# Optimization experiments

Measured on AMD Instinct MI355X. Metric: run time of the kernel, lower is better.

## Reference

```python
import jax, jax.numpy as jnp
import numpy as np

H, D = 16, 64  # num_attention_heads, attention_head_size
BASE = 10000.0

def _rope(q, k, seq_len):
    # RotaryPositionalEmbedding: inv_freq over arange(0, D, 2); emb = cat(freqs, freqs)
    inv_freq = 1.0 / (BASE ** (jnp.arange(0, D, 2, dtype=jnp.float32) / D))  # [D/2]=32
    pos = jnp.arange(seq_len, dtype=jnp.float32)
    freqs = jnp.outer(pos, inv_freq)            # [S, 32]; equals cos_emb[..., :d]
    cos, sin = jnp.cos(freqs), jnp.sin(freqs)   # [S, 32]
    d = D // 2                                   # 32: only first half of head dim rotated
    half = d // 2                                # 16: internal rotate-half within rot part
    def rot(x):  # x: [B, H, S, D]
        xr, xp = x[..., :d], x[..., d:]
        swapped = jnp.concatenate([xr[..., half:], xr[..., :half]], axis=-1)
        xr2 = xr * cos - swapped * sin
        return jnp.concatenate([xr2, xp], axis=-1)
    return rot(q), rot(k)

def setup_inputs() -> dict:
    key = jax.random.key(0)
    ks = jax.random.split(key, 9)
    B, S, E = 2, 2048, 1024
    std = 0.02  # initializer_range
    inp = {"hidden_states": jax.random.normal(ks[0], (B, S, E), jnp.float32)}
    for i, n in enumerate(["q", "k", "v", "d"]):
        inp[f"W{n}"] = jax.random.normal(ks[1 + 2 * i], (E, E), jnp.float32) * std
        inp[f"b{n}"] = jnp.zeros((E,), jnp.float32)
    return inp

def reference(hidden_states, Wq, bq, Wk, bk, Wv, bv, Wd, bd):
    B, S, E = hidden_states.shape
    def heads(x):  # [B,S,E] -> [B,H,S,D]
        return x.reshape(B, S, H, D).transpose(0, 2, 1, 3)
    q = heads(hidden_states @ Wq + bq)
    k = heads(hidden_states @ Wk + bk)
    v = heads(hidden_states @ Wv + bv)
    q, k = _rope(q, k, S)
    scores = jnp.einsum("bhqd,bhkd->bhqk", q, k) / jnp.sqrt(jnp.float32(D))
    causal = jnp.tril(jnp.ones((S, S), dtype=bool))
    scores = jnp.where(causal, scores, -jnp.inf)
    probs = jax.nn.softmax(scores, axis=-1)
    ctx = jnp.einsum("bhqk,bhkd->bhqd", probs, v)
    ctx = ctx.transpose(0, 2, 1, 3).reshape(B, S, E)
    return ctx @ Wd + bd
```

## Files before the change

### kernel.cpp

```cpp
#include <hip/hip_runtime.h>
#include <stdint.h>

typedef __bf16 bf8 __attribute__((ext_vector_type(8)));
typedef float f4 __attribute__((ext_vector_type(4)));
typedef float f16v __attribute__((ext_vector_type(16)));
typedef unsigned short us8 __attribute__((ext_vector_type(8)));
typedef unsigned short us4 __attribute__((ext_vector_type(4)));

#define MFMA16(a, b, c) __builtin_amdgcn_mfma_f32_16x16x32_bf16(a, b, c, 0, 0, 0)
#define MFMA32(a, b, c) __builtin_amdgcn_mfma_f32_32x32x16_bf16(a, b, c, 0, 0, 0)

__device__ __forceinline__ unsigned short f2b(float f) {
  union { float f; unsigned u; } x; x.f = f;
  unsigned u = x.u;
  u += 0x7fffu + ((u >> 16) & 1u);
  return (unsigned short)(u >> 16);
}

__device__ __forceinline__ unsigned pk2(float a, float b) {
  union { float f; unsigned u; } ua, ub; ua.f = a; ub.f = b;
  return __builtin_amdgcn_perm(ub.u + 0x8000u, ua.u + 0x8000u, 0x07060302u);
}

__device__ __forceinline__ void gload16(const void* g, void* l) {
  __builtin_amdgcn_global_load_lds(
      (const __attribute__((address_space(1))) void*)g,
      (__attribute__((address_space(3))) void*)l, 16, 0, 0);
}

__global__ __launch_bounds__(256) void cvt_bf16_kernel(
    const float* __restrict__ x, unsigned short* __restrict__ y) {
  int i = blockIdx.x * 256 + threadIdx.x;
  float4 v = ((const float4*)x)[i];
  us4 r = { f2b(v.x), f2b(v.y), f2b(v.z), f2b(v.w) };
  *(us4*)(y + (size_t)i * 4) = r;
}

__global__ __launch_bounds__(256) void transpose_cvt4_kernel(
    const float* __restrict__ W0, const float* __restrict__ W1,
    const float* __restrict__ W2, const float* __restrict__ W3,
    unsigned short* __restrict__ T0, unsigned short* __restrict__ T1,
    unsigned short* __restrict__ T2, unsigned short* __restrict__ T3) {
  const float* W; unsigned short* Wt;
  if (blockIdx.z == 0)      { W = W0; Wt = T0; }
  else if (blockIdx.z == 1) { W = W1; Wt = T1; }
  else if (blockIdx.z == 2) { W = W2; Wt = T2; }
  else                      { W = W3; Wt = T3; }
  __shared__ float tile[32][33];
  int tx = threadIdx.x & 31, ty = threadIdx.x >> 5;
  int kb = blockIdx.x * 32, nb = blockIdx.y * 32;
#pragma unroll
  for (int j = 0; j < 32; j += 8)
    tile[ty + j][tx] = W[(size_t)(kb + ty + j) * 1024 + nb + tx];
  __syncthreads();
#pragma unroll
  for (int j = 0; j < 32; j += 8)
    Wt[(size_t)(nb + ty + j) * 1024 + kb + tx] = f2b(tile[tx][ty + j]);
}

__global__ __launch_bounds__(256) void gemm_qkv_kernel(
    const unsigned short* __restrict__ X,
    const unsigned short* __restrict__ Wqt, const unsigned short* __restrict__ Wkt,
    const unsigned short* __restrict__ Wvt,
    const float* __restrict__ bq, const float* __restrict__ bk,
    const float* __restrict__ bv,
    unsigned short* __restrict__ Qo, unsigned short* __restrict__ Ko,
    unsigned short* __restrict__ Vo) {
  const unsigned short* Wt; const float* bias; unsigned short* out;
  if (blockIdx.z == 0)      { Wt = Wqt; bias = bq; out = Qo; }
  else if (blockIdx.z == 1) { Wt = Wkt; bias = bk; out = Ko; }
  else                      { Wt = Wvt; bias = bv; out = Vo; }

  __shared__ unsigned short As[128 * 32];
  __shared__ unsigned short Bs[128 * 32];
  const int t = threadIdx.x;
  const int wave = t >> 6, lane = t & 63, quad = lane >> 4, l16 = lane & 15;
  const int wm = (wave >> 1) * 64, wn = (wave & 1) * 64;
  const int m0 = blockIdx.y * 128, n0 = blockIdx.x * 128;

  f4 acc[4][4];
#pragma unroll
  for (int mi = 0; mi < 4; ++mi)
#pragma unroll
    for (int ni = 0; ni < 4; ++ni) acc[mi][ni] = (f4)0.0f;

  for (int k0 = 0; k0 < 1024; k0 += 32) {
    __syncthreads();
#pragma unroll
    for (int it = 0; it < 2; ++it) {
      int chunk = it * 256 + wave * 64 + lane;
      int row = chunk >> 2, c = chunk & 3;
      gload16(&X[(size_t)(m0 + row) * 1024 + k0 + c * 8],
              &As[(size_t)(it * 256 + wave * 64) * 8]);
      gload16(&Wt[(size_t)(n0 + row) * 1024 + k0 + c * 8],
              &Bs[(size_t)(it * 256 + wave * 64) * 8]);
    }
    __syncthreads();
    bf8 a[4], b[4];
#pragma unroll
    for (int mi = 0; mi < 4; ++mi)
      a[mi] = *(const bf8*)&As[(wm + mi * 16 + l16) * 32 + quad * 8];
#pragma unroll
    for (int ni = 0; ni < 4; ++ni)
      b[ni] = *(const bf8*)&Bs[(wn + ni * 16 + l16) * 32 + quad * 8];
#pragma unroll
    for (int mi = 0; mi < 4; ++mi)
#pragma unroll
      for (int ni = 0; ni < 4; ++ni)
        acc[mi][ni] = MFMA16(a[mi], b[ni], acc[mi][ni]);
  }

  float biasv[4];
#pragma unroll
  for (int ni = 0; ni < 4; ++ni) biasv[ni] = bias[n0 + wn + ni * 16 + l16];

  if (blockIdx.z < 2) {
    const float kr = 13.287712379549449f / 32.0f;
    const float f0 = exp2f(-(float)l16 * kr);
    const float f1 = exp2f(-(float)(l16 + 16) * kr);
    const float qs = (blockIdx.z == 0) ? 0.18033688011112042f : 1.0f;
#pragma unroll
    for (int mi = 0; mi < 4; ++mi) {
#pragma unroll
      for (int r = 0; r < 4; ++r) {
        int m = m0 + wm + mi * 16 + quad * 4 + r;
        float s = (float)(m & 2047);
        float s0, c0, s1, c1;
        __sincosf(s * f0, &s0, &c0);
        __sincosf(s * f1, &s1, &c1);
        float v0 = acc[mi][0][r] + biasv[0];
        float v1 = acc[mi][1][r] + biasv[1];
        acc[mi][0][r] = (v0 * c0 - v1 * s0) * qs;
        acc[mi][1][r] = (v1 * c1 - v0 * s1) * qs;
        acc[mi][2][r] = (acc[mi][2][r] + biasv[2]) * qs;
        acc[mi][3][r] = (acc[mi][3][r] + biasv[3]) * qs;
      }
    }
#pragma unroll
    for (int ni = 0; ni < 4; ++ni) {
      int n = n0 + wn + ni * 16 + l16;
      int h = n >> 6, d = n & 63;
#pragma unroll
      for (int mi = 0; mi < 4; ++mi) {
#pragma unroll
        for (int r = 0; r < 4; ++r) {
          int m = m0 + wm + mi * 16 + quad * 4 + r;
          int b_ = m >> 11, s = m & 2047;
          out[(size_t)(((b_ << 4) | h) * 2048 + s) * 64 + d] = f2b(acc[mi][ni][r]);
        }
      }
    }
  } else {
#pragma unroll
    for (int ni = 0; ni < 4; ++ni) {
      int n = n0 + wn + ni * 16 + l16;
      int h = n >> 6, d = n & 63;
#pragma unroll
      for (int mi = 0; mi < 4; ++mi) {
        int m = m0 + wm + mi * 16 + quad * 4;
        int b_ = m >> 11, s = m & 2047;
        us4 w = { f2b(acc[mi][ni][0] + biasv[ni]), f2b(acc[mi][ni][1] + biasv[ni]),
                  f2b(acc[mi][ni][2] + biasv[ni]), f2b(acc[mi][ni][3] + biasv[ni]) };
        *(us4*)&out[((size_t)(((b_ << 4) | h) * 64 + d)) * 2048 + s] = w;
      }
    }
  }
}

__global__ __launch_bounds__(256, 2) void flash_attn_kernel(
    const unsigned short* __restrict__ Q, const unsigned short* __restrict__ K,
    const unsigned short* __restrict__ Vt, unsigned short* __restrict__ ctx) {
  const int t = threadIdx.x;
  const int lane = t & 63;
  const int wave = t >> 6, l32 = lane & 31, hl = lane >> 5;

  const int id = blockIdx.x;
  const int bh = id & 31;
  const int j = id >> 5;
  const int qt = (j >> 3) ? (15 - (j & 7)) : (j & 7);
  const int qbase = qt * 128;
  const int b = bh >> 4, h = bh & 15;

  const unsigned short* Qh = Q + (size_t)bh * 2048 * 64;
  const unsigned short* Kh = K + (size_t)bh * 2048 * 64;
  const unsigned short* Vh = Vt + (size_t)bh * 64 * 2048;

  const int wrow0 = qbase + wave * 32;
  const int q = wrow0 + l32;

  bf8 qb[4];
#pragma unroll
  for (int c = 0; c < 4; ++c)
    qb[c] = *(const bf8*)&Qh[(size_t)q * 64 + c * 16 + hl * 8];

  f16v o0 = (f16v)0.0f, o1 = (f16v)0.0f;
  float mrow = -3e38f, lrow = 0.0f;
  const int nkw = (wrow0 >> 6) + 1;

  bf8 kfA[2][4], kfB[2][4], vf[2][4];

  auto loadK = [&](bf8 (&kf)[2][4], int k0) {
#pragma unroll
    for (int mt = 0; mt < 2; ++mt)
#pragma unroll
      for (int c = 0; c < 4; ++c)
        kf[mt][c] = *(const bf8*)&Kh[(size_t)(k0 + mt * 32 + l32) * 64 + c * 16 + hl * 8];
  };
  auto loadV = [&](int k0) {
#pragma unroll
    for (int dt = 0; dt < 2; ++dt)
#pragma unroll
      for (int c = 0; c < 4; ++c)
        vf[dt][c] = *(const bf8*)&Vh[(size_t)(dt * 32 + l32) * 2048 + k0 + c * 16 + hl * 8];
  };

  auto step = [&](int k0, bf8 (&kf)[2][4]) {
    f16v s0 = (f16v)0.0f, s1 = (f16v)0.0f;
#pragma unroll
    for (int c = 0; c < 4; ++c) {
      s0 = MFMA32(kf[0][c], qb[c], s0);
      s1 = MFMA32(kf[1][c], qb[c], s1);
    }
    if (k0 + 64 > wrow0) {
#pragma unroll
      for (int g = 0; g < 4; ++g)
#pragma unroll
        for (int i = 0; i < 4; ++i) {
          int kk = k0 + g * 8 + hl * 4 + i;
          if (kk > q) s0[g * 4 + i] = -3e38f;
          if (kk + 32 > q) s1[g * 4 + i] = -3e38f;
        }
    }
    float mx = fmaxf(s0[0], s1[0]);
#pragma unroll
    for (int i = 1; i < 16; ++i) mx = fmaxf(mx, fmaxf(s0[i], s1[i]));
    mx = fmaxf(mx, __shfl_xor(mx, 32));
    float mn = fmaxf(mrow, mx);
    float al = exp2f(mrow - mn);
    mrow = mn;
    uint2 pd2[8];
    float sum = 0.0f;
#pragma unroll
    for (int g = 0; g < 4; ++g) {
      float p0 = exp2f(s0[g * 4 + 0] - mn), p1 = exp2f(s0[g * 4 + 1] - mn);
      float p2 = exp2f(s0[g * 4 + 2] - mn), p3 = exp2f(s0[g * 4 + 3] - mn);
      sum += (p0 + p1) + (p2 + p3);
      pd2[g].x = pk2(p0, p1); pd2[g].y = pk2(p2, p3);
      float r0 = exp2f(s1[g * 4 + 0] - mn), r1 = exp2f(s1[g * 4 + 1] - mn);
      float r2 = exp2f(s1[g * 4 + 2] - mn), r3 = exp2f(s1[g * 4 + 3] - mn);
      sum += (r0 + r1) + (r2 + r3);
      pd2[4 + g].x = pk2(r0, r1); pd2[4 + g].y = pk2(r2, r3);
    }
#pragma unroll
    for (int i = 0; i < 16; ++i) { o0[i] *= al; o1[i] *= al; }
#pragma unroll
    for (int c = 0; c < 4; ++c) {
      uint2 lo = pd2[2 * c], hi = pd2[2 * c + 1];
      unsigned sx = hl ? lo.x : hi.x, sy = hl ? lo.y : hi.y;
      unsigned rx = __shfl_xor(sx, 32), ry = __shfl_xor(sy, 32);
      union { uint4 u; bf8 v; } fr;
      fr.u.x = hl ? rx : lo.x;
      fr.u.y = hl ? ry : lo.y;
      fr.u.z = hl ? hi.x : rx;
      fr.u.w = hl ? hi.y : ry;
      o0 = MFMA32(vf[0][c], fr.v, o0);
      o1 = MFMA32(vf[1][c], fr.v, o1);
    }
    sum += __shfl_xor(sum, 32);
    lrow = lrow * al + sum;
  };

  loadK(kfA, 0);
  int kt = 0;
  while (true) {
    loadV(kt * 64);
    if (kt + 1 < nkw) loadK(kfB, (kt + 1) * 64);
    step(kt * 64, kfA);
    ++kt; if (kt >= nkw) break;
    loadV(kt * 64);
    if (kt + 1 < nkw) loadK(kfA, (kt + 1) * 64);
    step(kt * 64, kfB);
    ++kt; if (kt >= nkw) break;
  }

  float inv = 1.0f / lrow;
#pragma unroll
  for (int g = 0; g < 4; ++g) {
    int d0 = g * 8 + hl * 4;
    us4 w0 = { f2b(o0[g * 4 + 0] * inv), f2b(o0[g * 4 + 1] * inv),
               f2b(o0[g * 4 + 2] * inv), f2b(o0[g * 4 + 3] * inv) };
    *(us4*)&ctx[((size_t)(b * 2048 + q)) * 1024 + h * 64 + d0] = w0;
    us4 w1 = { f2b(o1[g * 4 + 0] * inv), f2b(o1[g * 4 + 1] * inv),
               f2b(o1[g * 4 + 2] * inv), f2b(o1[g * 4 + 3] * inv) };
    *(us4*)&ctx[((size_t)(b * 2048 + q)) * 1024 + h * 64 + 32 + d0] = w1;
  }
}

__global__ __launch_bounds__(256) void gemm_out_kernel(
    const unsigned short* __restrict__ A,
    const unsigned short* __restrict__ Wt,
    const float* __restrict__ bias, float* __restrict__ out) {
  __shared__ unsigned short As[64 * 32];
  __shared__ unsigned short Bs[128 * 32];
  const int t = threadIdx.x;
  const int wave = t >> 6, lane = t & 63, quad = lane >> 4, l16 = lane & 15;
  const int wm = (wave & 1) * 32, wn = (wave >> 1) * 64;
  const int m0 = blockIdx.y * 64, n0 = blockIdx.x * 128;

  f4 acc[2][4];
#pragma unroll
  for (int mi = 0; mi < 2; ++mi)
#pragma unroll
    for (int ni = 0; ni < 4; ++ni) acc[mi][ni] = (f4)0.0f;

  for (int k0 = 0; k0 < 1024; k0 += 32) {
    __syncthreads();
    {
      int chunk = wave * 64 + lane;
      int row = chunk >> 2, c = chunk & 3;
      gload16(&A[(size_t)(m0 + row) * 1024 + k0 + c * 8],
              &As[(size_t)(wave * 64) * 8]);
#pragma unroll
      for (int it = 0; it < 2; ++it) {
        int ch = it * 256 + wave * 64 + lane;
        int rw = ch >> 2, cc = ch & 3;
        gload16(&Wt[(size_t)(n0 + rw) * 1024 + k0 + cc * 8],
                &Bs[(size_t)(it * 256 + wave * 64) * 8]);
      }
    }
    __syncthreads();
    bf8 a[2], b[4];
#pragma unroll
    for (int mi = 0; mi < 2; ++mi)
      a[mi] = *(const bf8*)&As[(wm + mi * 16 + l16) * 32 + quad * 8];
#pragma unroll
    for (int ni = 0; ni < 4; ++ni)
      b[ni] = *(const bf8*)&Bs[(wn + ni * 16 + l16) * 32 + quad * 8];
#pragma unroll
    for (int mi = 0; mi < 2; ++mi)
#pragma unroll
      for (int ni = 0; ni < 4; ++ni)
        acc[mi][ni] = MFMA16(a[mi], b[ni], acc[mi][ni]);
  }
#pragma unroll
  for (int ni = 0; ni < 4; ++ni) {
    int n = n0 + wn + ni * 16 + l16;
    float bv_ = bias[n];
#pragma unroll
    for (int mi = 0; mi < 2; ++mi) {
#pragma unroll
      for (int r = 0; r < 4; ++r) {
        int m = m0 + wm + mi * 16 + quad * 4 + r;
        out[(size_t)m * 1024 + n] = acc[mi][ni][r] + bv_;
      }
    }
  }
}

extern "C" void kernel_launch(void* const* d_in, const int* in_sizes, int n_in,
                              void* d_out, int out_size, void* d_ws, size_t ws_size,
                              hipStream_t stream) {
  const float* hidden = (const float*)d_in[0];
  const float* Wq = (const float*)d_in[1];
  const float* bq = (const float*)d_in[2];
  const float* Wk = (const float*)d_in[3];
  const float* bk = (const float*)d_in[4];
  const float* Wv = (const float*)d_in[5];
  const float* bv = (const float*)d_in[6];
  const float* Wd = (const float*)d_in[7];
  const float* bd = (const float*)d_in[8];
  float* out = (float*)d_out;

  char* ws = (char*)d_ws;
  unsigned short* Xb  = (unsigned short*)(ws);
  unsigned short* Wqt = (unsigned short*)(ws + ( 8ull << 20));
  unsigned short* Wkt = (unsigned short*)(ws + (10ull << 20));
  unsigned short* Wvt = (unsigned short*)(ws + (12ull << 20));
  unsigned short* Wdt = (unsigned short*)(ws + (14ull << 20));
  unsigned short* Qb  = (unsigned short*)(ws + (16ull << 20));
  unsigned short* Kb  = (unsigned short*)(ws + (24ull << 20));
  unsigned short* Vb  = (unsigned short*)(ws + (32ull << 20));
  unsigned short* Cb  = (unsigned short*)(ws + (40ull << 20));

  cvt_bf16_kernel<<<4096, 256, 0, stream>>>(hidden, Xb);
  transpose_cvt4_kernel<<<dim3(32, 32, 4), 256, 0, stream>>>(
      Wq, Wk, Wv, Wd, Wqt, Wkt, Wvt, Wdt);
  gemm_qkv_kernel<<<dim3(8, 32, 3), 256, 0, stream>>>(
      Xb, Wqt, Wkt, Wvt, bq, bk, bv, Qb, Kb, Vb);
  flash_attn_kernel<<<512, 256, 0, stream>>>(Qb, Kb, Vb, Cb);
  gemm_out_kernel<<<dim3(8, 64), 256, 0, stream>>>(Cb, Wdt, bd, out);
}
```

Before: 225.3 us.

## Split flash-attention KV range across wave pairs and merge partials in LDS

The attention kernel now uses 64-row query tiles and 1024 blocks. Within each block, two wave pairs split the key tiles by parity (split-K), and their partial max, sum and output are merged through shared memory at the end. The aim is more parallelism and better load balance across CUs on the causal triangle, with the launch bound raised to 4 blocks per CU for occupancy. In exchange it adds an LDS merge, a block barrier, and register pressure from the occupancy hint, and each K/V tile is still loaded separately by each wave.

```diff
diff --git a/kernel.cpp b/kernel.cpp
--- a/kernel.cpp
+++ b/kernel.cpp
@@ -167,25 +167,28 @@
   }
 }
 
-__global__ __launch_bounds__(256, 2) void flash_attn_kernel(
+__global__ __launch_bounds__(256, 4) void flash_attn_kernel(
     const unsigned short* __restrict__ Q, const unsigned short* __restrict__ K,
     const unsigned short* __restrict__ Vt, unsigned short* __restrict__ ctx) {
+  __shared__ float Mrg[2][64][34];
+
   const int t = threadIdx.x;
   const int lane = t & 63;
   const int wave = t >> 6, l32 = lane & 31, hl = lane >> 5;
+  const int qsub = wave >> 1, khalf = wave & 1;
 
   const int id = blockIdx.x;
   const int bh = id & 31;
   const int j = id >> 5;
-  const int qt = (j >> 3) ? (15 - (j & 7)) : (j & 7);
-  const int qbase = qt * 128;
+  const int g = (j < 16) ? j : 47 - j;
+  const int qbase = g * 64;
   const int b = bh >> 4, h = bh & 15;
 
   const unsigned short* Qh = Q + (size_t)bh * 2048 * 64;
   const unsigned short* Kh = K + (size_t)bh * 2048 * 64;
   const unsigned short* Vh = Vt + (size_t)bh * 64 * 2048;
 
-  const int wrow0 = qbase + wave * 32;
+  const int wrow0 = qbase + qsub * 32;
   const int q = wrow0 + l32;
 
   bf8 qb[4];
@@ -195,7 +198,6 @@
 
   f16v o0 = (f16v)0.0f, o1 = (f16v)0.0f;
   float mrow = -3e38f, lrow = 0.0f;
-  const int nkw = (wrow0 >> 6) + 1;
 
   bf8 kfA[2][4], kfB[2][4], vf[2][4];
 
@@ -223,12 +225,12 @@
     }
     if (k0 + 64 > wrow0) {
 #pragma unroll
-      for (int g = 0; g < 4; ++g)
+      for (int gg = 0; gg < 4; ++gg)
 #pragma unroll
         for (int i = 0; i < 4; ++i) {
-          int kk = k0 + g * 8 + hl * 4 + i;
-          if (kk > q) s0[g * 4 + i] = -3e38f;
-          if (kk + 32 > q) s1[g * 4 + i] = -3e38f;
+          int kk = k0 + gg * 8 + hl * 4 + i;
+          if (kk > q) s0[gg * 4 + i] = -3e38f;
+          if (kk + 32 > q) s1[gg * 4 + i] = -3e38f;
         }
     }
     float mx = fmaxf(s0[0], s1[0]);
@@ -241,15 +243,15 @@
     uint2 pd2[8];
     float sum = 0.0f;
 #pragma unroll
-    for (int g = 0; g < 4; ++g) {
-      float p0 = exp2f(s0[g * 4 + 0] - mn), p1 = exp2f(s0[g * 4 + 1] - mn);
-      float p2 = exp2f(s0[g * 4 + 2] - mn), p3 = exp2f(s0[g * 4 + 3] - mn);
+    for (int gg = 0; gg < 4; ++gg) {
+      float p0 = exp2f(s0[gg * 4 + 0] - mn), p1 = exp2f(s0[gg * 4 + 1] - mn);
+      float p2 = exp2f(s0[gg * 4 + 2] - mn), p3 = exp2f(s0[gg * 4 + 3] - mn);
       sum += (p0 + p1) + (p2 + p3);
-      pd2[g].x = pk2(p0, p1); pd2[g].y = pk2(p2, p3);
-      float r0 = exp2f(s1[g * 4 + 0] - mn), r1 = exp2f(s1[g * 4 + 1] - mn);
-      float r2 = exp2f(s1[g * 4 + 2] - mn), r3 = exp2f(s1[g * 4 + 3] - mn);
+      pd2[gg].x = pk2(p0, p1); pd2[gg].y = pk2(p2, p3);
+      float r0 = exp2f(s1[gg * 4 + 0] - mn), r1 = exp2f(s1[gg * 4 + 1] - mn);
+      float r2 = exp2f(s1[gg * 4 + 2] - mn), r3 = exp2f(s1[gg * 4 + 3] - mn);
       sum += (r0 + r1) + (r2 + r3);
-      pd2[4 + g].x = pk2(r0, r1); pd2[4 + g].y = pk2(r2, r3);
+      pd2[4 + gg].x = pk2(r0, r1); pd2[4 + gg].y = pk2(r2, r3);
     }
 #pragma unroll
     for (int i = 0; i < 16; ++i) { o0[i] *= al; o1[i] *= al; }
@@ -270,29 +272,51 @@
     lrow = lrow * al + sum;
   };
 
-  loadK(kfA, 0);
-  int kt = 0;
-  while (true) {
-    loadV(kt * 64);
-    if (kt + 1 < nkw) loadK(kfB, (kt + 1) * 64);
-    step(kt * 64, kfA);
-    ++kt; if (kt >= nkw) break;
-    loadV(kt * 64);
-    if (kt + 1 < nkw) loadK(kfA, (kt + 1) * 64);
-    step(kt * 64, kfB);
-    ++kt; if (kt >= nkw) break;
-  }
-
-  float inv = 1.0f / lrow;
-#pragma unroll
-  for (int g = 0; g < 4; ++g) {
-    int d0 = g * 8 + hl * 4;
-    us4 w0 = { f2b(o0[g * 4 + 0] * inv), f2b(o0[g * 4 + 1] * inv),
-               f2b(o0[g * 4 + 2] * inv), f2b(o0[g * 4 + 3] * inv) };
-    *(us4*)&ctx[((size_t)(b * 2048 + q)) * 1024 + h * 64 + d0] = w0;
-    us4 w1 = { f2b(o1[g * 4 + 0] * inv), f2b(o1[g * 4 + 1] * inv),
-               f2b(o1[g * 4 + 2] * inv), f2b(o1[g * 4 + 3] * inv) };
-    *(us4*)&ctx[((size_t)(b * 2048 + q)) * 1024 + h * 64 + 32 + d0] = w1;
+  int kt = khalf;
+  if (kt <= g) {
+    loadK(kfA, kt * 64);
+    while (true) {
+      loadV(kt * 64);
+      if (kt + 2 <= g) loadK(kfB, (kt + 2) * 64);
+      step(kt * 64, kfA);
+      kt += 2; if (kt > g) break;
+      loadV(kt * 64);
+      if (kt + 2 <= g) loadK(kfA, (kt + 2) * 64);
+      step(kt * 64, kfB);
+      kt += 2; if (kt > g) break;
+    }
+  }
+
+  if (khalf == 1) {
+#pragma unroll
+    for (int i = 0; i < 16; ++i) {
+      Mrg[qsub][lane][i] = o0[i];
+      Mrg[qsub][lane][16 + i] = o1[i];
+    }
+    Mrg[qsub][lane][32] = mrow;
+    Mrg[qsub][lane][33] = lrow;
+  }
+  __syncthreads();
+  if (khalf == 0) {
+    float m1 = Mrg[qsub][lane][32], l1 = Mrg[qsub][lane][33];
+    float mm = fmaxf(mrow, m1);
+    float a0 = exp2f(mrow - mm), a1 = exp2f(m1 - mm);
+    float inv = 1.0f / (lrow * a0 + l1 * a1);
+    a0 *= inv; a1 *= inv;
+#pragma unroll
+    for (int gg = 0; gg < 4; ++gg) {
+      int d0 = gg * 8 + hl * 4;
+      us4 w0 = { f2b(o0[gg * 4 + 0] * a0 + Mrg[qsub][lane][gg * 4 + 0] * a1),
+                 f2b(o0[gg * 4 + 1] * a0 + Mrg[qsub][lane][gg * 4 + 1] * a1),
+                 f2b(o0[gg * 4 + 2] * a0 + Mrg[qsub][lane][gg * 4 + 2] * a1),
+                 f2b(o0[gg * 4 + 3] * a0 + Mrg[qsub][lane][gg * 4 + 3] * a1) };
+      *(us4*)&ctx[((size_t)(b * 2048 + q)) * 1024 + h * 64 + d0] = w0;
+      us4 w1 = { f2b(o1[gg * 4 + 0] * a0 + Mrg[qsub][lane][16 + gg * 4 + 0] * a1),
+                 f2b(o1[gg * 4 + 1] * a0 + Mrg[qsub][lane][16 + gg * 4 + 1] * a1),
+                 f2b(o1[gg * 4 + 2] * a0 + Mrg[qsub][lane][16 + gg * 4 + 2] * a1),
+                 f2b(o1[gg * 4 + 3] * a0 + Mrg[qsub][lane][16 + gg * 4 + 3] * a1) };
+      *(us4*)&ctx[((size_t)(b * 2048 + q)) * 1024 + h * 64 + 32 + d0] = w1;
+    }
   }
 }
 
@@ -387,6 +411,6 @@
       Wq, Wk, Wv, Wd, Wqt, Wkt, Wvt, Wdt);
   gemm_qkv_kernel<<<dim3(8, 32, 3), 256, 0, stream>>>(
       Xb, Wqt, Wkt, Wvt, bq, bk, bv, Qb, Kb, Vb);
-  flash_attn_kernel<<<512, 256, 0, stream>>>(Qb, Kb, Vb, Cb);
+  flash_attn_kernel<<<1024, 256, 0, stream>>>(Qb, Kb, Vb, Cb);
   gemm_out_kernel<<<dim3(8, 64), 256, 0, stream>>>(Cb, Wdt, bd, out);
 }
```

New measurement: 345.4 us. 1.53x slower.
